# Kernel tuning notes

Measured on AMD Instinct MI355X. Metric: run time of the kernel, lower is better.

The kernel has to match this reference:

```python
import jax, jax.numpy as jnp
import numpy as np

N, E, F, H, D, G, C = 50000, 800000, 128, 4, 64, 32, 3
NEG_SLOPE = 0.2  # PyG GATConv default negative_slope


def _gat_layer(x, src, dst, W, a_src, a_dst, b, heads, concat):
    """PyG GATConv (eval mode): gather -> leaky-relu score -> per-dst softmax -> scatter-add."""
    n = x.shape[0]
    h = (x @ W).reshape(n, heads, -1)                    # [N, H, D]
    al_s = jnp.sum(h * a_src, axis=-1)                   # [N, H]
    al_d = jnp.sum(h * a_dst, axis=-1)                   # [N, H]
    e = jax.nn.leaky_relu(al_s[src] + al_d[dst], NEG_SLOPE)   # [E, H]
    m = jax.ops.segment_max(e, dst, num_segments=n)      # segment softmax (self-loops ensure non-empty)
    ex = jnp.exp(e - m[dst])
    s = jax.ops.segment_sum(ex, dst, num_segments=n)
    alpha = ex / s[dst]                                  # [E, H]
    msg = h[src] * alpha[:, :, None]                     # [E, H, D]
    out = jax.ops.segment_sum(msg, dst, num_segments=n)  # [N, H, D]
    out = out.reshape(n, -1) if concat else out.mean(axis=1)
    return out + b, alpha


def setup_inputs() -> dict:
    key = jax.random.key(0)
    ks = jax.random.split(key, 20)
    sc = 0.1
    inp = {
        "x": jax.random.normal(ks[0], (N, F), jnp.float32),
        "edge_index": jax.random.randint(ks[1], (2, E), 0, N, dtype=jnp.int64),
        "batch": jnp.sort(jax.random.randint(ks[2], (N,), 0, G, dtype=jnp.int64)),
        "W1": jax.random.normal(ks[3], (F, H * D), jnp.float32) * sc,
        "as1": jax.random.normal(ks[4], (H, D), jnp.float32) * sc,
        "ad1": jax.random.normal(ks[5], (H, D), jnp.float32) * sc,
        "b1": jax.random.normal(ks[6], (H * D,), jnp.float32) * sc,
        "W2": jax.random.normal(ks[7], (H * D, H * D), jnp.float32) * sc,
        "as2": jax.random.normal(ks[8], (H, D), jnp.float32) * sc,
        "ad2": jax.random.normal(ks[9], (H, D), jnp.float32) * sc,
        "b2": jax.random.normal(ks[10], (H * D,), jnp.float32) * sc,
        "W3": jax.random.normal(ks[11], (H * D, D), jnp.float32) * sc,
        "as3": jax.random.normal(ks[12], (1, D), jnp.float32) * sc,
        "ad3": jax.random.normal(ks[13], (1, D), jnp.float32) * sc,
        "b3": jax.random.normal(ks[14], (D,), jnp.float32) * sc,
        "Wc1": jax.random.normal(ks[15], (D, D // 2), jnp.float32) * sc,
        "bc1": jax.random.normal(ks[16], (D // 2,), jnp.float32) * sc,
        "Wc2": jax.random.normal(ks[17], (D // 2, C), jnp.float32) * sc,
        "bc2": jax.random.normal(ks[18], (C,), jnp.float32) * sc,
    }
    return inp


def reference(x, edge_index, batch, W1, as1, ad1, b1, W2, as2, ad2, b2,
              W3, as3, ad3, b3, Wc1, bc1, Wc2, bc2):
    n = x.shape[0]
    loops = jnp.arange(n, dtype=edge_index.dtype)
    ei = jnp.concatenate([edge_index, jnp.stack([loops, loops])], axis=1)  # add_self_loops=True
    src, dst = ei[0], ei[1]

    h1, att1 = _gat_layer(x, src, dst, W1, as1, ad1, b1, H, True)
    h1 = jax.nn.elu(h1)  # dropout is identity in eval
    h2, att2 = _gat_layer(h1, src, dst, W2, as2, ad2, b2, H, True)
    h2 = jax.nn.elu(h2)
    h3, att3 = _gat_layer(h2, src, dst, W3, as3, ad3, b3, 1, False)

    # global_mean_pool over graphs
    sums = jax.ops.segment_sum(h3, batch, num_segments=G)
    cnts = jax.ops.segment_sum(jnp.ones((n,), h3.dtype), batch, num_segments=G)
    pooled = sums / jnp.maximum(cnts, 1.0)[:, None]

    hid = jax.nn.relu(pooled @ Wc1 + bc1)
    out = hid @ Wc2 + bc2  # [G, C]
    return out, att1, att2, att3
```

## Files before the change

### kernel.cpp

```cpp
#include <hip/hip_runtime.h>
#include <hip/hip_bf16.h>

#define N_NODES 50000
#define N_EDGES 800000
#define EP (N_EDGES + N_NODES)
#define F_IN 128
#define DH 64
#define HD 256
#define NG 32
#define NC 3
#define SCB 782
#define AGG_BLOCKS 2048

typedef float f32x4 __attribute__((ext_vector_type(4)));
typedef __bf16 bf16x8 __attribute__((ext_vector_type(8)));
typedef unsigned short u16x4 __attribute__((ext_vector_type(4)));
typedef unsigned short u16x8 __attribute__((ext_vector_type(8)));

__device__ inline float wave_max(float v) {
#pragma unroll
  for (int o = 32; o > 0; o >>= 1) v = fmaxf(v, __shfl_xor(v, o));
  return v;
}
__device__ inline float wave_sum(float v) {
#pragma unroll
  for (int o = 32; o > 0; o >>= 1) v += __shfl_xor(v, o);
  return v;
}
__device__ inline int wave_isum(int v) {
#pragma unroll
  for (int o = 32; o > 0; o >>= 1) v += __shfl_xor(v, o);
  return v;
}
__device__ inline int wave_iscan(int v, int lane) {
#pragma unroll
  for (int o = 1; o < 64; o <<= 1) {
    int t = __shfl_up(v, o);
    if (lane >= o) v += t;
  }
  return v;
}

__device__ inline unsigned short bf_hi(float f) {
  unsigned u = __float_as_uint(f);
  return (unsigned short)((u + 0x7FFFu + ((u >> 16) & 1u)) >> 16);
}
__device__ inline float4 bf4_to_f4(u16x4 v) {
  float4 r;
  r.x = __uint_as_float((unsigned)v.x << 16);
  r.y = __uint_as_float((unsigned)v.y << 16);
  r.z = __uint_as_float((unsigned)v.z << 16);
  r.w = __uint_as_float((unsigned)v.w << 16);
  return r;
}

__device__ inline int src_of(const int* __restrict__ ei, int e) {
  int s = (e < N_EDGES) ? ei[e] : (e - N_EDGES);
  if ((unsigned)s >= N_NODES) s = 0;
  return s;
}
__device__ inline int dst_of(const int* __restrict__ ei, int e) {
  int d = (e < N_EDGES) ? ei[N_EDGES + e] : (e - N_EDGES);
  if ((unsigned)d >= N_NODES) d = 0;
  return d;
}

__global__ void k_wsplit(const float* __restrict__ W,
                         unsigned short* __restrict__ wt_hi,
                         unsigned short* __restrict__ wt_lo,
                         int K, int Nn) {
  int idx = blockIdx.x * blockDim.x + threadIdx.x;
  if (idx >= K * Nn) return;
  int k = idx / Nn, n = idx % Nn;
  float v = W[idx];
  unsigned short h = bf_hi(v);
  float hf = __uint_as_float((unsigned)h << 16);
  unsigned short l = bf_hi(v - hf);
  wt_hi[(size_t)n * K + k] = h;
  wt_lo[(size_t)n * K + k] = l;
}

template <int NT>
__global__ __launch_bounds__(256) void k_gemm_mfma(
    const float* __restrict__ A,
    const unsigned short* __restrict__ Wt_hi,
    const unsigned short* __restrict__ Wt_lo,
    unsigned short* __restrict__ Cb,
    int M, int Nn, int K,
    const float* __restrict__ a_s, const float* __restrict__ a_d,
    float* __restrict__ al_s, float* __restrict__ al_d, int heads) {
  __shared__ unsigned short Ah[64 * 64];
  __shared__ unsigned short Al[64 * 64];
  __shared__ unsigned short Bh[NT * 64 * 64];
  __shared__ unsigned short Bl[NT * 64 * 64];
  __shared__ float prs[2][64], prd[2][64];

  int t = threadIdx.x;
  int lane = t & 63, w = t >> 6;
  int wr = w & 1, wc = w >> 1;
  int bm0 = blockIdx.y * 64, bn0 = blockIdx.x * (64 * NT);

  f32x4 acc[NT][2][2];
#pragma unroll
  for (int nt = 0; nt < NT; ++nt)
#pragma unroll
    for (int i = 0; i < 2; ++i)
#pragma unroll
      for (int j = 0; j < 2; ++j) acc[nt][i][j] = (f32x4){0.f, 0.f, 0.f, 0.f};

  int ar = t >> 2, cq = t & 3;
  int swzA = (ar & 7) << 4;
  int bcol = t >> 2, kq = t & 3;
  int swzB = (bcol & 7) << 4;

  for (int k0 = 0; k0 < K; k0 += 64) {
    {
      int grow = bm0 + ar;
      float4 v[4];
      if (grow < M) {
        const float* ap = A + (size_t)grow * K + k0 + cq * 4;
#pragma unroll
        for (int i = 0; i < 4; ++i) v[i] = *(const float4*)(ap + i * 16);
      } else {
#pragma unroll
        for (int i = 0; i < 4; ++i) v[i] = make_float4(0.f, 0.f, 0.f, 0.f);
      }
#pragma unroll
      for (int i = 0; i < 4; ++i) {
        float f0 = v[i].x, f1 = v[i].y, f2 = v[i].z, f3 = v[i].w;
        u16x4 h4, l4;
        h4.x = bf_hi(f0); l4.x = bf_hi(f0 - __uint_as_float((unsigned)h4.x << 16));
        h4.y = bf_hi(f1); l4.y = bf_hi(f1 - __uint_as_float((unsigned)h4.y << 16));
        h4.z = bf_hi(f2); l4.z = bf_hi(f2 - __uint_as_float((unsigned)h4.z << 16));
        h4.w = bf_hi(f3); l4.w = bf_hi(f3 - __uint_as_float((unsigned)h4.w << 16));
        int kbyte = cq * 8 + i * 32;
        int off = ar * 128 + ((kbyte & 0x70) ^ swzA) + (kbyte & 15);
        *(u16x4*)((char*)Ah + off) = h4;
        *(u16x4*)((char*)Al + off) = l4;
      }
    }
#pragma unroll
    for (int nt = 0; nt < NT; ++nt) {
      const unsigned short* bh = Wt_hi + (size_t)(bn0 + nt * 64 + bcol) * K + k0 + kq * 16;
      const unsigned short* bl = Wt_lo + (size_t)(bn0 + nt * 64 + bcol) * K + k0 + kq * 16;
      u16x8 h0 = *(const u16x8*)bh;
      u16x8 h1 = *(const u16x8*)(bh + 8);
      u16x8 l0 = *(const u16x8*)bl;
      u16x8 l1 = *(const u16x8*)(bl + 8);
      int kb0 = kq * 32, kb1 = kq * 32 + 16;
      int off0 = nt * 8192 + bcol * 128 + (kb0 ^ swzB);
      int off1 = nt * 8192 + bcol * 128 + (kb1 ^ swzB);
      *(u16x8*)((char*)Bh + off0) = h0;
      *(u16x8*)((char*)Bh + off1) = h1;
      *(u16x8*)((char*)Bl + off0) = l0;
      *(u16x8*)((char*)Bl + off1) = l1;
    }
    __syncthreads();
#pragma unroll
    for (int ks = 0; ks < 2; ++ks) {
      bf16x8 fah[2], fal[2];
      int kbyte = ks * 64 + (lane >> 4) * 16;
#pragma unroll
      for (int fr = 0; fr < 2; ++fr) {
        int row = wr * 32 + fr * 16 + (lane & 15);
        int off = row * 128 + (kbyte ^ ((row & 7) << 4));
        fah[fr] = *(const bf16x8*)((const char*)Ah + off);
        fal[fr] = *(const bf16x8*)((const char*)Al + off);
      }
#pragma unroll
      for (int nt = 0; nt < NT; ++nt) {
        bf16x8 fbh[2], fbl[2];
#pragma unroll
        for (int fc = 0; fc < 2; ++fc) {
          int col = wc * 32 + fc * 16 + (lane & 15);
          int off = nt * 8192 + col * 128 + (kbyte ^ ((col & 7) << 4));
          fbh[fc] = *(const bf16x8*)((const char*)Bh + off);
          fbl[fc] = *(const bf16x8*)((const char*)Bl + off);
        }
#pragma unroll
        for (int fr = 0; fr < 2; ++fr)
#pragma unroll
          for (int fc = 0; fc < 2; ++fc) {
            acc[nt][fr][fc] = __builtin_amdgcn_mfma_f32_16x16x32_bf16(fah[fr], fbh[fc], acc[nt][fr][fc], 0, 0, 0);
            acc[nt][fr][fc] = __builtin_amdgcn_mfma_f32_16x16x32_bf16(fah[fr], fbl[fc], acc[nt][fr][fc], 0, 0, 0);
            acc[nt][fr][fc] = __builtin_amdgcn_mfma_f32_16x16x32_bf16(fal[fr], fbh[fc], acc[nt][fr][fc], 0, 0, 0);
          }
      }
    }
    __syncthreads();
  }
#pragma unroll
  for (int nt = 0; nt < NT; ++nt)
#pragma unroll
    for (int fr = 0; fr < 2; ++fr)
#pragma unroll
      for (int r = 0; r < 4; ++r) {
        int row = bm0 + wr * 32 + fr * 16 + (lane >> 4) * 4 + r;
        if (row < M) {
#pragma unroll
          for (int fc = 0; fc < 2; ++fc)
            Cb[(size_t)row * Nn + bn0 + nt * 64 + wc * 32 + fc * 16 + (lane & 15)] =
                bf_hi(acc[nt][fr][fc][r]);
        }
      }
  if (heads) {
#pragma unroll
    for (int nt = 0; nt < NT; ++nt) {
      int hh = blockIdx.x * NT + nt;
      int cw = wc * 32 + (lane & 15);
      float asv[2], adv[2];
#pragma unroll
      for (int fc = 0; fc < 2; ++fc) {
        asv[fc] = a_s[hh * 64 + cw + fc * 16];
        adv[fc] = a_d[hh * 64 + cw + fc * 16];
      }
#pragma unroll
      for (int fr = 0; fr < 2; ++fr)
#pragma unroll
        for (int r = 0; r < 4; ++r) {
          float ps = acc[nt][fr][0][r] * asv[0] + acc[nt][fr][1][r] * asv[1];
          float pd = acc[nt][fr][0][r] * adv[0] + acc[nt][fr][1][r] * adv[1];
#pragma unroll
          for (int o = 1; o < 16; o <<= 1) {
            ps += __shfl_xor(ps, o);
            pd += __shfl_xor(pd, o);
          }
          if ((lane & 15) == 0) {
            int rl = wr * 32 + fr * 16 + (lane >> 4) * 4 + r;
            prs[wc][rl] = ps;
            prd[wc][rl] = pd;
          }
        }
      __syncthreads();
      if (t < 64) {
        int grow = bm0 + t;
        if (grow < M) {
          al_s[(size_t)grow * heads + hh] = prs[0][t] + prs[1][t];
          al_d[(size_t)grow * heads + hh] = prd[0][t] + prd[1][t];
        }
      }
      __syncthreads();
    }
  }
}

__global__ void k_count(const int* __restrict__ ei, int* __restrict__ counts) {
  int e = blockIdx.x * blockDim.x + threadIdx.x;
  if (e >= EP) return;
  atomicAdd(&counts[dst_of(ei, e)], 1);
}
__global__ void k_scan_a(const int* __restrict__ counts, int* __restrict__ part) {
  int lane = threadIdx.x;
  int i = blockIdx.x * 64 + lane;
  int v = (i < N_NODES) ? counts[i] : 0;
  v = wave_isum(v);
  if (lane == 0) part[blockIdx.x] = v;
}
__global__ void k_scan_b(const int* __restrict__ part, int* __restrict__ partpref) {
  int lane = threadIdx.x;
  int carry = 0;
  for (int base = 0; base < SCB; base += 64) {
    int i = base + lane;
    int v = (i < SCB) ? part[i] : 0;
    int inc = wave_iscan(v, lane);
    if (i < SCB) partpref[i] = carry + inc - v;
    carry += __shfl(inc, 63);
  }
  if (lane == 0) partpref[SCB] = carry;
}
__global__ void k_scan_c(const int* __restrict__ counts, const int* __restrict__ partpref,
                         int* __restrict__ row_ptr, int* __restrict__ cursor) {
  int b = blockIdx.x, lane = threadIdx.x;
  int i = b * 64 + lane;
  int v = (i < N_NODES) ? counts[i] : 0;
  int inc = wave_iscan(v, lane);
  int excl = partpref[b] + inc - v;
  if (i < N_NODES) { row_ptr[i] = excl; cursor[i] = excl; }
  if (i == N_NODES - 1) row_ptr[N_NODES] = excl + v;
}
__global__ void k_scatter(const int* __restrict__ ei, int* __restrict__ cursor,
                          int* __restrict__ eidx, int* __restrict__ srcs) {
  int e = blockIdx.x * blockDim.x + threadIdx.x;
  if (e >= EP) return;
  int pos = atomicAdd(&cursor[dst_of(ei, e)], 1);
  if ((unsigned)pos < EP) { eidx[pos] = e; srcs[pos] = src_of(ei, e); }
}

__global__ __launch_bounds__(256) void k_aggregate4(
    const float* __restrict__ al_s, const float* __restrict__ al_d,
    const int* __restrict__ eidx, const int* __restrict__ srcs,
    const int* __restrict__ row_ptr,
    const unsigned short* __restrict__ h, const float* __restrict__ bias,
    float* __restrict__ xout, float* __restrict__ att) {
  __shared__ float aplane[4][4][65];
  __shared__ int   splane[4][64];
  int lane = threadIdx.x & 63;
  int wid = threadIdx.x >> 6;
  int wgid = blockIdx.x * 4 + wid;
  int nwaves = gridDim.x * 4;
  float4 b4 = *(const float4*)(bias + lane * 4);
  int hsel = lane >> 4;
  const unsigned short* hL = h + lane * 4;
  for (int n = wgid; n < N_NODES; n += nwaves) {
    int beg = row_ptr[n], end = row_ptr[n + 1];
    if (beg < 0) beg = 0;
    if (end > EP) end = EP;
    float4 ad4 = *(const float4*)(al_d + (size_t)n * 4);
    float m0 = -1e30f, m1 = -1e30f, m2 = -1e30f, m3 = -1e30f;
    float s0 = 0.f, s1 = 0.f, s2 = 0.f, s3 = 0.f;
    for (int i = beg + lane; i < end; i += 64) {
      int sl = srcs[i];
      if ((unsigned)sl >= N_NODES) sl = 0;
      float4 a4 = *(const float4*)(al_s + (size_t)sl * 4);
      float e0 = a4.x + ad4.x; e0 = e0 > 0.f ? e0 : 0.2f * e0; e0 = (e0 == e0) ? e0 : 0.f;
      float e1 = a4.y + ad4.y; e1 = e1 > 0.f ? e1 : 0.2f * e1; e1 = (e1 == e1) ? e1 : 0.f;
      float e2 = a4.z + ad4.z; e2 = e2 > 0.f ? e2 : 0.2f * e2; e2 = (e2 == e2) ? e2 : 0.f;
      float e3 = a4.w + ad4.w; e3 = e3 > 0.f ? e3 : 0.2f * e3; e3 = (e3 == e3) ? e3 : 0.f;
      float nm;
      nm = fmaxf(m0, e0); s0 = s0 * __expf(m0 - nm) + __expf(e0 - nm); m0 = nm;
      nm = fmaxf(m1, e1); s1 = s1 * __expf(m1 - nm) + __expf(e1 - nm); m1 = nm;
      nm = fmaxf(m2, e2); s2 = s2 * __expf(m2 - nm) + __expf(e2 - nm); m2 = nm;
      nm = fmaxf(m3, e3); s3 = s3 * __expf(m3 - nm) + __expf(e3 - nm); m3 = nm;
    }
    float M0 = wave_max(m0), M1 = wave_max(m1), M2 = wave_max(m2), M3 = wave_max(m3);
    s0 *= __expf(m0 - M0); s1 *= __expf(m1 - M1);
    s2 *= __expf(m2 - M2); s3 *= __expf(m3 - M3);
    s0 = wave_sum(s0); s1 = wave_sum(s1); s2 = wave_sum(s2); s3 = wave_sum(s3);
    float i0 = s0 > 0.f ? 1.f / s0 : 0.f;
    float i1 = s1 > 0.f ? 1.f / s1 : 0.f;
    float i2 = s2 > 0.f ? 1.f / s2 : 0.f;
    float i3 = s3 > 0.f ? 1.f / s3 : 0.f;
    float4 ac0 = {0.f, 0.f, 0.f, 0.f}, ac1 = {0.f, 0.f, 0.f, 0.f};
    float4 ac2 = {0.f, 0.f, 0.f, 0.f}, ac3 = {0.f, 0.f, 0.f, 0.f};
    for (int c = beg; c < end; c += 64) {
      int i = c + lane;
      float4 av = {0.f, 0.f, 0.f, 0.f};
      int sl = 0;
      if (i < end) {
        sl = srcs[i];
        if ((unsigned)sl >= N_NODES) sl = 0;
        float4 a4 = *(const float4*)(al_s + (size_t)sl * 4);
        float e0 = a4.x + ad4.x; e0 = e0 > 0.f ? e0 : 0.2f * e0; e0 = (e0 == e0) ? e0 : 0.f;
        float e1 = a4.y + ad4.y; e1 = e1 > 0.f ? e1 : 0.2f * e1; e1 = (e1 == e1) ? e1 : 0.f;
        float e2 = a4.z + ad4.z; e2 = e2 > 0.f ? e2 : 0.2f * e2; e2 = (e2 == e2) ? e2 : 0.f;
        float e3 = a4.w + ad4.w; e3 = e3 > 0.f ? e3 : 0.2f * e3; e3 = (e3 == e3) ? e3 : 0.f;
        av.x = __expf(e0 - M0) * i0;
        av.y = __expf(e1 - M1) * i1;
        av.z = __expf(e2 - M2) * i2;
        av.w = __expf(e3 - M3) * i3;
        *(float4*)(att + (size_t)eidx[i] * 4) = av;
      }
      aplane[wid][0][lane] = av.x;
      aplane[wid][1][lane] = av.y;
      aplane[wid][2][lane] = av.z;
      aplane[wid][3][lane] = av.w;
      splane[wid][lane] = sl;
      asm volatile("s_waitcnt lgkmcnt(0)" ::: "memory");
      int cnt = end - c; if (cnt > 64) cnt = 64;
      int j = 0;
      for (; j + 4 <= cnt; j += 4) {
        int q0 = splane[wid][j + 0], q1 = splane[wid][j + 1];
        int q2 = splane[wid][j + 2], q3 = splane[wid][j + 3];
        float a0 = aplane[wid][hsel][j + 0], a1 = aplane[wid][hsel][j + 1];
        float a2 = aplane[wid][hsel][j + 2], a3 = aplane[wid][hsel][j + 3];
        float4 h0 = bf4_to_f4(*(const u16x4*)(hL + (size_t)q0 * HD));
        float4 h1 = bf4_to_f4(*(const u16x4*)(hL + (size_t)q1 * HD));
        float4 h2 = bf4_to_f4(*(const u16x4*)(hL + (size_t)q2 * HD));
        float4 h3 = bf4_to_f4(*(const u16x4*)(hL + (size_t)q3 * HD));
        ac0.x += a0 * h0.x; ac0.y += a0 * h0.y; ac0.z += a0 * h0.z; ac0.w += a0 * h0.w;
        ac1.x += a1 * h1.x; ac1.y += a1 * h1.y; ac1.z += a1 * h1.z; ac1.w += a1 * h1.w;
        ac2.x += a2 * h2.x; ac2.y += a2 * h2.y; ac2.z += a2 * h2.z; ac2.w += a2 * h2.w;
        ac3.x += a3 * h3.x; ac3.y += a3 * h3.y; ac3.z += a3 * h3.z; ac3.w += a3 * h3.w;
      }
      for (; j < cnt; ++j) {
        int q = splane[wid][j];
        float a = aplane[wid][hsel][j];
        float4 hv = bf4_to_f4(*(const u16x4*)(hL + (size_t)q * HD));
        ac0.x += a * hv.x; ac0.y += a * hv.y; ac0.z += a * hv.z; ac0.w += a * hv.w;
      }
      asm volatile("s_waitcnt lgkmcnt(0)" ::: "memory");
    }
    float4 o;
    o.x = (ac0.x + ac1.x) + (ac2.x + ac3.x) + b4.x;
    o.y = (ac0.y + ac1.y) + (ac2.y + ac3.y) + b4.y;
    o.z = (ac0.z + ac1.z) + (ac2.z + ac3.z) + b4.z;
    o.w = (ac0.w + ac1.w) + (ac2.w + ac3.w) + b4.w;
    o.x = o.x > 0.f ? o.x : expm1f(o.x);
    o.y = o.y > 0.f ? o.y : expm1f(o.y);
    o.z = o.z > 0.f ? o.z : expm1f(o.z);
    o.w = o.w > 0.f ? o.w : expm1f(o.w);
    *(float4*)(xout + (size_t)n * HD + lane * 4) = o;
  }
}

__global__ __launch_bounds__(256) void k_aggregate1(
    const float* __restrict__ al_s, const float* __restrict__ al_d,
    const int* __restrict__ eidx, const int* __restrict__ srcs,
    const int* __restrict__ row_ptr,
    const unsigned short* __restrict__ h, float* __restrict__ out_acc,
    float* __restrict__ att) {
  __shared__ float aplane[4][64];
  __shared__ int   splane[4][64];
  int lane = threadIdx.x & 63;
  int wid = threadIdx.x >> 6;
  int wgid = blockIdx.x * 4 + wid;
  int nwaves = gridDim.x * 4;
  const unsigned short* hL = h + lane;
  for (int n = wgid; n < N_NODES; n += nwaves) {
    int beg = row_ptr[n], end = row_ptr[n + 1];
    if (beg < 0) beg = 0;
    if (end > EP) end = EP;
    float ad = al_d[n];
    float m = -1e30f, ssum = 0.f;
    for (int i = beg + lane; i < end; i += 64) {
      int sl = srcs[i];
      if ((unsigned)sl >= N_NODES) sl = 0;
      float e = al_s[sl] + ad;
      e = e > 0.f ? e : 0.2f * e;
      e = (e == e) ? e : 0.f;
      float nm = fmaxf(m, e);
      ssum = ssum * __expf(m - nm) + __expf(e - nm);
      m = nm;
    }
    float M = wave_max(m);
    ssum *= __expf(m - M);
    ssum = wave_sum(ssum);
    float inv = (ssum > 0.f) ? 1.f / ssum : 0.f;
    float a0c = 0.f, a1c = 0.f, a2c = 0.f, a3c = 0.f;
    for (int c = beg; c < end; c += 64) {
      int i = c + lane;
      float av = 0.f;
      int sl = 0;
      if (i < end) {
        sl = srcs[i];
        if ((unsigned)sl >= N_NODES) sl = 0;
        float e = al_s[sl] + ad;
        e = e > 0.f ? e : 0.2f * e;
        e = (e == e) ? e : 0.f;
        av = __expf(e - M) * inv;
        att[eidx[i]] = av;
      }
      aplane[wid][lane] = av;
      splane[wid][lane] = sl;
      asm volatile("s_waitcnt lgkmcnt(0)" ::: "memory");
      int cnt = end - c; if (cnt > 64) cnt = 64;
      int j = 0;
      for (; j + 4 <= cnt; j += 4) {
        int q0 = splane[wid][j + 0], q1 = splane[wid][j + 1];
        int q2 = splane[wid][j + 2], q3 = splane[wid][j + 3];
        float a0 = aplane[wid][j + 0], a1 = aplane[wid][j + 1];
        float a2 = aplane[wid][j + 2], a3 = aplane[wid][j + 3];
        float h0 = __uint_as_float((unsigned)hL[(size_t)q0 * DH] << 16);
        float h1 = __uint_as_float((unsigned)hL[(size_t)q1 * DH] << 16);
        float h2 = __uint_as_float((unsigned)hL[(size_t)q2 * DH] << 16);
        float h3 = __uint_as_float((unsigned)hL[(size_t)q3 * DH] << 16);
        a0c += a0 * h0; a1c += a1 * h1; a2c += a2 * h2; a3c += a3 * h3;
      }
      for (; j < cnt; ++j) {
        int q = splane[wid][j];
        float a = aplane[wid][j];
        a0c += a * __uint_as_float((unsigned)hL[(size_t)q * DH] << 16);
      }
      asm volatile("s_waitcnt lgkmcnt(0)" ::: "memory");
    }
    out_acc[(size_t)n * DH + lane] = (a0c + a1c) + (a2c + a3c);
  }
}

__global__ void k_gstart(const int* __restrict__ batch, int* __restrict__ gstart) {
  int i = blockIdx.x * blockDim.x + threadIdx.x;
  if (i >= N_NODES) return;
  int g = batch[i] & (NG - 1);
  if (i == 0) gstart[g] = 0;
  else {
    int gp = batch[i - 1] & (NG - 1);
    if (g != gp) gstart[g] = i;
  }
}
__global__ void k_gfix(int* __restrict__ gstart) {
  if (threadIdx.x != 0 || blockIdx.x != 0) return;
  gstart[NG] = N_NODES;
  for (int g = NG - 1; g >= 0; --g)
    if (gstart[g] < 0) gstart[g] = gstart[g + 1];
}

__global__ __launch_bounds__(1024) void k_pool2(const float* __restrict__ acc,
                                                const float* __restrict__ b3,
                                                const int* __restrict__ gstart,
                                                float* __restrict__ pooled,
                                                float* __restrict__ cnt) {
  __shared__ float red[16][DH];
  int g = blockIdx.x;
  int lo = gstart[g], hi = gstart[g + 1];
  int d = threadIdx.x & (DH - 1);
  int sub = threadIdx.x >> 6;
  float s = 0.f;
  for (int n = lo + sub; n < hi; n += 16)
    s += acc[(size_t)n * DH + d];
  red[sub][d] = s;
  __syncthreads();
  if (sub == 0) {
    float tot = 0.f;
#pragma unroll
    for (int r = 0; r < 16; ++r) tot += red[r][d];
    int c = hi - lo;
    pooled[g * DH + d] = tot + (float)c * b3[d];
    if (d == 0) cnt[g] = (float)c;
  }
}

__global__ void k_mlp(const float* __restrict__ pooled, const float* __restrict__ cnt,
                      const float* __restrict__ Wc1, const float* __restrict__ bc1,
                      const float* __restrict__ Wc2, const float* __restrict__ bc2,
                      float* __restrict__ out) {
  __shared__ float hid[NG * 32];
  int t = threadIdx.x;
  for (int idx = t; idx < NG * 32; idx += blockDim.x) {
    int g = idx / 32, j = idx % 32;
    float invc = 1.f / fmaxf(cnt[g], 1.f);
    float a = bc1[j];
    for (int d = 0; d < DH; ++d)
      a += pooled[g * DH + d] * invc * Wc1[d * 32 + j];
    hid[idx] = a > 0.f ? a : 0.f;
  }
  __syncthreads();
  for (int idx = t; idx < NG * NC; idx += blockDim.x) {
    int g = idx / NC, c = idx % NC;
    float a = bc2[c];
    for (int j = 0; j < 32; ++j)
      a += hid[g * 32 + j] * Wc2[j * NC + c];
    out[idx] = a;
  }
}

extern "C" void kernel_launch(void* const* d_in, const int* in_sizes, int n_in,
                              void* d_out, int out_size, void* d_ws, size_t ws_size,
                              hipStream_t stream) {
  const float* x   = (const float*)d_in[0];
  const int* ei    = (const int*)d_in[1];
  const int* batch = (const int*)d_in[2];
  const float* W1  = (const float*)d_in[3];
  const float* as1 = (const float*)d_in[4];
  const float* ad1 = (const float*)d_in[5];
  const float* b1  = (const float*)d_in[6];
  const float* W2  = (const float*)d_in[7];
  const float* as2 = (const float*)d_in[8];
  const float* ad2 = (const float*)d_in[9];
  const float* b2  = (const float*)d_in[10];
  const float* W3  = (const float*)d_in[11];
  const float* as3 = (const float*)d_in[12];
  const float* ad3 = (const float*)d_in[13];
  const float* b3  = (const float*)d_in[14];
  const float* Wc1 = (const float*)d_in[15];
  const float* bc1 = (const float*)d_in[16];
  const float* Wc2 = (const float*)d_in[17];
  const float* bc2 = (const float*)d_in[18];
  float* out = (float*)d_out;

  char* w = (char*)d_ws;
  unsigned short* h_bf = (unsigned short*)(w + 0);
  float* out_acc = (float*)(w + 51200000);
  float* al_s    = (float*)(w + 102400000);
  float* al_d    = (float*)(w + 103200000);
  unsigned short* wt_hi = (unsigned short*)(w + 104000000);
  unsigned short* wt_lo = (unsigned short*)(w + 104200000);
  int*   counts  = (int*)(w + 117600000);
  int*   cursor  = (int*)(w + 117800000);
  int*   row_ptr = (int*)(w + 118000000);
  int*   eidx    = (int*)(w + 118200064);
  int*   srcs    = (int*)(w + 121600064);
  int*   part    = (int*)(w + 125000064);
  int*   partpref= (int*)(w + 125003264);
  float* pooled  = (float*)(w + 125006464);
  float* gcnt    = (float*)(w + 125014656);
  int*   gstart  = (int*)(w + 125014784);

  const int EB = (EP + 255) / 256;

  hipMemsetAsync(counts, 0, N_NODES * sizeof(int), stream);
  hipMemsetAsync(eidx, 0, EP * sizeof(int), stream);
  hipMemsetAsync(srcs, 0, EP * sizeof(int), stream);
  hipMemsetAsync(gstart, 0xFF, (NG + 1) * sizeof(int), stream);

  k_count<<<EB, 256, 0, stream>>>(ei, counts);
  k_scan_a<<<SCB, 64, 0, stream>>>(counts, part);
  k_scan_b<<<1, 64, 0, stream>>>(part, partpref);
  k_scan_c<<<SCB, 64, 0, stream>>>(counts, partpref, row_ptr, cursor);
  k_scatter<<<EB, 256, 0, stream>>>(ei, cursor, eidx, srcs);
  k_gstart<<<(N_NODES + 255) / 256, 256, 0, stream>>>(batch, gstart);
  k_gfix<<<1, 64, 0, stream>>>(gstart);

  float* att1 = out + 96;
  float* att2 = out + 3400096;
  float* att3 = out + 6800096;

  dim3 gh(HD / 128, (N_NODES + 63) / 64);
  dim3 gd(1, (N_NODES + 63) / 64);

  k_wsplit<<<(F_IN * HD + 255) / 256, 256, 0, stream>>>(W1, wt_hi, wt_lo, F_IN, HD);
  k_gemm_mfma<2><<<gh, 256, 0, stream>>>(x, wt_hi, wt_lo, h_bf, N_NODES, HD, F_IN,
                                         as1, ad1, al_s, al_d, 4);
  k_aggregate4<<<AGG_BLOCKS, 256, 0, stream>>>(al_s, al_d, eidx, srcs, row_ptr,
                                               h_bf, b1, out_acc, att1);

  k_wsplit<<<(HD * HD + 255) / 256, 256, 0, stream>>>(W2, wt_hi, wt_lo, HD, HD);
  k_gemm_mfma<2><<<gh, 256, 0, stream>>>(out_acc, wt_hi, wt_lo, h_bf, N_NODES, HD, HD,
                                         as2, ad2, al_s, al_d, 4);
  k_aggregate4<<<AGG_BLOCKS, 256, 0, stream>>>(al_s, al_d, eidx, srcs, row_ptr,
                                               h_bf, b2, out_acc, att2);

  k_wsplit<<<(HD * DH + 255) / 256, 256, 0, stream>>>(W3, wt_hi, wt_lo, HD, DH);
  k_gemm_mfma<1><<<gd, 256, 0, stream>>>(out_acc, wt_hi, wt_lo, h_bf, N_NODES, DH, HD,
                                         as3, ad3, al_s, al_d, 1);
  k_aggregate1<<<AGG_BLOCKS, 256, 0, stream>>>(al_s, al_d, eidx, srcs, row_ptr,
                                               h_bf, out_acc, att3);

  k_pool2<<<NG, 1024, 0, stream>>>(out_acc, b3, gstart, pooled, gcnt);
  k_mlp<<<1, 256, 0, stream>>>(pooled, gcnt, Wc1, bc1, Wc2, bc2, out);
}
```

Before: 576.5 us.

## Store inter-layer activations as bf16 and skip A-split MFMAs in later GEMMs

```diff
diff --git a/kernel.cpp b/kernel.cpp
--- a/kernel.cpp
+++ b/kernel.cpp
@@ -80,9 +80,9 @@
   wt_lo[(size_t)n * K + k] = l;
 }
 
-template <int NT>
+template <int NT, bool SPLITA>
 __global__ __launch_bounds__(256) void k_gemm_mfma(
-    const float* __restrict__ A,
+    const void* __restrict__ Av,
     const unsigned short* __restrict__ Wt_hi,
     const unsigned short* __restrict__ Wt_lo,
     unsigned short* __restrict__ Cb,
@@ -90,7 +90,7 @@
     const float* __restrict__ a_s, const float* __restrict__ a_d,
     float* __restrict__ al_s, float* __restrict__ al_d, int heads) {
   __shared__ unsigned short Ah[64 * 64];
-  __shared__ unsigned short Al[64 * 64];
+  __shared__ unsigned short Al[SPLITA ? 64 * 64 : 64];
   __shared__ unsigned short Bh[NT * 64 * 64];
   __shared__ unsigned short Bl[NT * 64 * 64];
   __shared__ float prs[2][64], prd[2][64];
@@ -114,7 +114,8 @@
   int swzB = (bcol & 7) << 4;
 
   for (int k0 = 0; k0 < K; k0 += 64) {
-    {
+    if (SPLITA) {
+      const float* A = (const float*)Av;
       int grow = bm0 + ar;
       float4 v[4];
       if (grow < M) {
@@ -138,6 +139,21 @@
         *(u16x4*)((char*)Ah + off) = h4;
         *(u16x4*)((char*)Al + off) = l4;
       }
+    } else {
+      const unsigned short* A = (const unsigned short*)Av;
+      int grow = bm0 + ar;
+      u16x8 a0, a1;
+      if (grow < M) {
+        const unsigned short* ap = A + (size_t)grow * K + k0 + cq * 16;
+        a0 = *(const u16x8*)ap;
+        a1 = *(const u16x8*)(ap + 8);
+      } else {
+        a0 = (u16x8){0, 0, 0, 0, 0, 0, 0, 0};
+        a1 = (u16x8){0, 0, 0, 0, 0, 0, 0, 0};
+      }
+      int kb0 = cq * 32, kb1 = cq * 32 + 16;
+      *(u16x8*)((char*)Ah + ar * 128 + (kb0 ^ swzA)) = a0;
+      *(u16x8*)((char*)Ah + ar * 128 + (kb1 ^ swzA)) = a1;
     }
 #pragma unroll
     for (int nt = 0; nt < NT; ++nt) {
@@ -165,7 +181,7 @@
         int row = wr * 32 + fr * 16 + (lane & 15);
         int off = row * 128 + (kbyte ^ ((row & 7) << 4));
         fah[fr] = *(const bf16x8*)((const char*)Ah + off);
-        fal[fr] = *(const bf16x8*)((const char*)Al + off);
+        if (SPLITA) fal[fr] = *(const bf16x8*)((const char*)Al + off);
       }
 #pragma unroll
       for (int nt = 0; nt < NT; ++nt) {
@@ -183,7 +199,8 @@
           for (int fc = 0; fc < 2; ++fc) {
             acc[nt][fr][fc] = __builtin_amdgcn_mfma_f32_16x16x32_bf16(fah[fr], fbh[fc], acc[nt][fr][fc], 0, 0, 0);
             acc[nt][fr][fc] = __builtin_amdgcn_mfma_f32_16x16x32_bf16(fah[fr], fbl[fc], acc[nt][fr][fc], 0, 0, 0);
-            acc[nt][fr][fc] = __builtin_amdgcn_mfma_f32_16x16x32_bf16(fal[fr], fbh[fc], acc[nt][fr][fc], 0, 0, 0);
+            if (SPLITA)
+              acc[nt][fr][fc] = __builtin_amdgcn_mfma_f32_16x16x32_bf16(fal[fr], fbh[fc], acc[nt][fr][fc], 0, 0, 0);
           }
       }
     }
@@ -291,7 +308,7 @@
     const int* __restrict__ eidx, const int* __restrict__ srcs,
     const int* __restrict__ row_ptr,
     const unsigned short* __restrict__ h, const float* __restrict__ bias,
-    float* __restrict__ xout, float* __restrict__ att) {
+    unsigned short* __restrict__ xout, float* __restrict__ att) {
   __shared__ float aplane[4][4][65];
   __shared__ int   splane[4][64];
   int lane = threadIdx.x & 63;
@@ -389,7 +406,9 @@
     o.y = o.y > 0.f ? o.y : expm1f(o.y);
     o.z = o.z > 0.f ? o.z : expm1f(o.z);
     o.w = o.w > 0.f ? o.w : expm1f(o.w);
-    *(float4*)(xout + (size_t)n * HD + lane * 4) = o;
+    u16x4 ob;
+    ob.x = bf_hi(o.x); ob.y = bf_hi(o.y); ob.z = bf_hi(o.z); ob.w = bf_hi(o.w);
+    *(u16x4*)(xout + (size_t)n * HD + lane * 4) = ob;
   }
 }
 
@@ -558,28 +577,27 @@
   float* out = (float*)d_out;
 
   char* w = (char*)d_ws;
-  unsigned short* h_bf = (unsigned short*)(w + 0);
-  float* out_acc = (float*)(w + 51200000);
-  float* al_s    = (float*)(w + 102400000);
-  float* al_d    = (float*)(w + 103200000);
-  unsigned short* wt_hi = (unsigned short*)(w + 104000000);
-  unsigned short* wt_lo = (unsigned short*)(w + 104200000);
-  int*   counts  = (int*)(w + 117600000);
-  int*   cursor  = (int*)(w + 117800000);
-  int*   row_ptr = (int*)(w + 118000000);
-  int*   eidx    = (int*)(w + 118200064);
-  int*   srcs    = (int*)(w + 121600064);
-  int*   part    = (int*)(w + 125000064);
-  int*   partpref= (int*)(w + 125003264);
-  float* pooled  = (float*)(w + 125006464);
-  float* gcnt    = (float*)(w + 125014656);
-  int*   gstart  = (int*)(w + 125014784);
+  unsigned short* h_bf  = (unsigned short*)(w + 0);
+  unsigned short* x2_bf = (unsigned short*)(w + 25600000);
+  float* acc3    = (float*)(w + 51200000);
+  float* al_s    = (float*)(w + 64000000);
+  float* al_d    = (float*)(w + 64800000);
+  unsigned short* wt_hi = (unsigned short*)(w + 65600000);
+  unsigned short* wt_lo = (unsigned short*)(w + 65800000);
+  int*   counts  = (int*)(w + 66000000);
+  int*   cursor  = (int*)(w + 66200000);
+  int*   row_ptr = (int*)(w + 66400000);
+  int*   eidx    = (int*)(w + 66600064);
+  int*   srcs    = (int*)(w + 70000064);
+  int*   part    = (int*)(w + 73400064);
+  int*   partpref= (int*)(w + 73403264);
+  float* pooled  = (float*)(w + 73406464);
+  float* gcnt    = (float*)(w + 73414656);
+  int*   gstart  = (int*)(w + 73414784);
 
   const int EB = (EP + 255) / 256;
 
   hipMemsetAsync(counts, 0, N_NODES * sizeof(int), stream);
-  hipMemsetAsync(eidx, 0, EP * sizeof(int), stream);
-  hipMemsetAsync(srcs, 0, EP * sizeof(int), stream);
   hipMemsetAsync(gstart, 0xFF, (NG + 1) * sizeof(int), stream);
 
   k_count<<<EB, 256, 0, stream>>>(ei, counts);
@@ -598,23 +616,26 @@
   dim3 gd(1, (N_NODES + 63) / 64);
 
   k_wsplit<<<(F_IN * HD + 255) / 256, 256, 0, stream>>>(W1, wt_hi, wt_lo, F_IN, HD);
-  k_gemm_mfma<2><<<gh, 256, 0, stream>>>(x, wt_hi, wt_lo, h_bf, N_NODES, HD, F_IN,
-                                         as1, ad1, al_s, al_d, 4);
+  k_gemm_mfma<2, true><<<gh, 256, 0, stream>>>(x, wt_hi, wt_lo, h_bf,
+                                               N_NODES, HD, F_IN,
+                                               as1, ad1, al_s, al_d, 4);
   k_aggregate4<<<AGG_BLOCKS, 256, 0, stream>>>(al_s, al_d, eidx, srcs, row_ptr,
-                                               h_bf, b1, out_acc, att1);
+                                               h_bf, b1, x2_bf, att1);
 
   k_wsplit<<<(HD * HD + 255) / 256, 256, 0, stream>>>(W2, wt_hi, wt_lo, HD, HD);
-  k_gemm_mfma<2><<<gh, 256, 0, stream>>>(out_acc, wt_hi, wt_lo, h_bf, N_NODES, HD, HD,
-                                         as2, ad2, al_s, al_d, 4);
+  k_gemm_mfma<2, false><<<gh, 256, 0, stream>>>(x2_bf, wt_hi, wt_lo, h_bf,
+                                                N_NODES, HD, HD,
+                                                as2, ad2, al_s, al_d, 4);
   k_aggregate4<<<AGG_BLOCKS, 256, 0, stream>>>(al_s, al_d, eidx, srcs, row_ptr,
-                                               h_bf, b2, out_acc, att2);
+                                               h_bf, b2, x2_bf, att2);
 
   k_wsplit<<<(HD * DH + 255) / 256, 256, 0, stream>>>(W3, wt_hi, wt_lo, HD, DH);
-  k_gemm_mfma<1><<<gd, 256, 0, stream>>>(out_acc, wt_hi, wt_lo, h_bf, N_NODES, DH, HD,
-                                         as3, ad3, al_s, al_d, 1);
+  k_gemm_mfma<1, false><<<gd, 256, 0, stream>>>(x2_bf, wt_hi, wt_lo, h_bf,
+                                                N_NODES, DH, HD,
+                                                as3, ad3, al_s, al_d, 1);
   k_aggregate1<<<AGG_BLOCKS, 256, 0, stream>>>(al_s, al_d, eidx, srcs, row_ptr,
-                                               h_bf, out_acc, att3);
-
-  k_pool2<<<NG, 1024, 0, stream>>>(out_acc, b3, gstart, pooled, gcnt);
+                                               h_bf, acc3, att3);
+
+  k_pool2<<<NG, 1024, 0, stream>>>(acc3, b3, gstart, pooled, gcnt);
   k_mlp<<<1, 256, 0, stream>>>(pooled, gcnt, Wc1, bc1, Wc2, bc2, out);
 }
```

After: 549.4 us. -4.7%, faster.
